# Kernel tuning notes

Measured on AMD Instinct MI355X. Metric: run time of the kernel, lower is better.

Reference implementation:

```python
import jax, jax.numpy as jnp
import numpy as np

N_NODES = 50000
N_EDGES = 800000
EMB = 128
N_LAYERS = 2
BN_EPS = 1e-5


def setup_inputs() -> dict:
    key = jax.random.key(0)
    ks = jax.random.split(key, 16)
    N, E, D, L = N_NODES, N_EDGES, EMB, N_LAYERS
    x = jax.random.randint(ks[0], (N, 2), 0, 3)
    edge_index = jax.random.randint(ks[1], (2, E), 0, N)
    edge_attr = jax.random.randint(ks[2], (E, 2), 0, 3)
    batch = jnp.zeros((N,), dtype=jnp.int32)
    s = 0.1
    xemb1 = jax.random.normal(ks[3], (120, D)) * s   # atom-type embedding
    xemb2 = jax.random.normal(ks[4], (3, D)) * s     # chirality embedding
    e1 = jax.random.normal(ks[5], (L, 7, D)) * s     # bond-type embedding per layer
    e2 = jax.random.normal(ks[6], (L, 3, D)) * s     # bond-direction embedding per layer
    W1 = jax.random.normal(ks[7], (L, D, 2 * D)) * s
    b1 = jnp.zeros((L, 2 * D))
    W2 = jax.random.normal(ks[8], (L, 2 * D, D)) * s
    b2 = jnp.zeros((L, D))
    gamma = jnp.ones((L, D))
    beta = jnp.zeros((L, D))
    return {"x": x, "edge_index": edge_index, "edge_attr": edge_attr, "batch": batch,
            "xemb1": xemb1, "xemb2": xemb2, "e1": e1, "e2": e2,
            "W1": W1, "b1": b1, "W2": W2, "b2": b2, "gamma": gamma, "beta": beta}


def _gnn_forward(x, edge_index, edge_attr, xemb1, xemb2, e1, e2, W1, b1, W2, b2, gamma, beta):
    N = x.shape[0]
    # add self loops; self-loop edge_attr = [4, 0]
    loop = jnp.arange(N, dtype=edge_index.dtype)
    src = jnp.concatenate([edge_index[0], loop])
    dst = jnp.concatenate([edge_index[1], loop])
    loop_attr = jnp.concatenate([jnp.full((N, 1), 4, dtype=edge_attr.dtype),
                                 jnp.zeros((N, 1), dtype=edge_attr.dtype)], axis=1)
    ea = jnp.concatenate([edge_attr, loop_attr], axis=0)  # [E+N, 2]

    # input node embedding
    h = xemb1[x[:, 0]] + xemb2[x[:, 1]]  # [N, D]

    for l in range(N_LAYERS):
        eemb = e1[l][ea[:, 0]] + e2[l][ea[:, 1]]      # [E+N, D]
        msg = h[src] + eemb                            # gather + edge fuse
        agg = jax.ops.segment_sum(msg, dst, num_segments=N)  # scatter-add
        # GIN update MLP: Linear -> ReLU -> Linear
        h2 = jax.nn.relu(agg @ W1[l] + b1[l]) @ W2[l] + b2[l]
        # BatchNorm1d (training mode: biased batch stats)
        mu = jnp.mean(h2, axis=0)
        var = jnp.mean(jnp.square(h2 - mu), axis=0)
        h2 = gamma[l] * (h2 - mu) * jax.lax.rsqrt(var + BN_EPS) + beta[l]
        # dropout(relu) for non-final layers; drop_ratio=0 -> identity dropout
        h = h2 if l == N_LAYERS - 1 else jax.nn.relu(h2)
    return h  # JK='last'


def reference(x, edge_index, edge_attr, batch, xemb1, xemb2, e1, e2, W1, b1, W2, b2, gamma, beta):
    return _gnn_forward(x, edge_index, edge_attr, xemb1, xemb2, e1, e2, W1, b1, W2, b2, gamma, beta)
```

## Files before the change

### kernel.cpp

```cpp
#include <hip/hip_runtime.h>
#include <stdint.h>

#define N_NODES 50000
#define N_EDGES 800000
#define EMB 128
#define NPAD 50176
#define MBLK 392
#define BN_EPS 1e-5f
#define SENT_KEY ((N_NODES << 5) | 21)
#define NODES_PER_XCD 6250
#define XCHUNK 2048
#define NCHUNKS ((N_EDGES + XCHUNK - 1) / XCHUNK)
#define PBLK 196

typedef __attribute__((ext_vector_type(8))) short short8;
typedef __attribute__((ext_vector_type(4))) float f32x4;

__device__ __forceinline__ unsigned short f2bf(float f) {
    unsigned int u = __float_as_uint(f);
    u += 0x7fffu + ((u >> 16) & 1u);
    return (unsigned short)(u >> 16);
}
__device__ __forceinline__ float bflo(unsigned int v) { return __uint_as_float(v << 16); }
__device__ __forceinline__ float bfhi(unsigned int v) { return __uint_as_float(v & 0xffff0000u); }
__device__ __forceinline__ unsigned int packbf(float lo, float hi) {
    return (unsigned int)f2bf(lo) | ((unsigned int)f2bf(hi) << 16);
}

__global__ void k_prep(const int* __restrict__ x, const float* __restrict__ xe1,
                       const float* __restrict__ xe2, unsigned int* __restrict__ h,
                       const float* __restrict__ W1, const float* __restrict__ W2,
                       unsigned short* __restrict__ w1t, unsigned short* __restrict__ w2t,
                       int* __restrict__ deg,
                       const int* __restrict__ ei, const int* __restrict__ ea,
                       int* __restrict__ keyv) {
    int idx = blockIdx.x * 256 + threadIdx.x;
    int i = idx >> 6, j = idx & 63;
    if (i < N_NODES) {
        int a = x[2 * i], c = x[2 * i + 1];
        float2 va = *(const float2*)(xe1 + a * EMB + j * 2);
        float2 vb = *(const float2*)(xe2 + c * EMB + j * 2);
        h[i * 64 + j] = packbf(va.x + vb.x, va.y + vb.y);
    } else if (i == N_NODES) {
        h[(size_t)i * 64 + j] = 0u;
    }
    if (idx < 4 * 32768) {
        int sec = idx >> 15, q = idx & 32767;
        if (sec < 2) {
            int r = q >> 8, c = q & 255;
            w1t[sec * 32768 + c * 128 + r] = f2bf(W1[sec * 32768 + q]);
        } else {
            int s = sec - 2;
            int r = q >> 7, c = q & 127;
            w2t[s * 32768 + c * 256 + r] = f2bf(W2[s * 32768 + q]);
        }
    }
    if (idx < N_EDGES) {
        int2 aa = *(const int2*)(ea + 2 * idx);
        keyv[idx] = (ei[idx] << 5) | (aa.x * 3 + aa.y);
        atomicAdd(&deg[ei[N_EDGES + idx]], 1);
    }
}

__global__ void k_alloc(const int* __restrict__ deg, int* __restrict__ gcur,
                        int* __restrict__ offs, int* __restrict__ cursor,
                        int* __restrict__ keys, int* __restrict__ bcnt) {
    __shared__ int wbase[4];
    __shared__ int lc[8];
    int tid = threadIdx.x, lane = tid & 63, wid = tid >> 6;
    if (tid < 8) lc[tid] = 0;
    int i = blockIdx.x * 256 + tid;
    int d = (i < N_NODES) ? deg[i] : 0;
    int pd = (d + 15) & ~15;
    int s = pd;
#pragma unroll
    for (int off = 1; off < 64; off <<= 1) {
        int t = __shfl_up(s, off);
        if (lane >= off) s += t;
    }
    if (lane == 63) wbase[wid] = s;
    __syncthreads();
    if (tid == 0) {
        int t0 = wbase[0], t1 = wbase[1], t2 = wbase[2], t3 = wbase[3];
        int b = atomicAdd(gcur, t0 + t1 + t2 + t3);
        wbase[0] = b; wbase[1] = b + t0; wbase[2] = b + t0 + t1; wbase[3] = b + t0 + t1 + t2;
    }
    __syncthreads();
    if (i < N_NODES) {
        int o = wbase[wid] + s - pd;
        offs[i] = o;
        cursor[i] = o;
        for (int j = d; j < pd; ++j) keys[o + j] = SENT_KEY;
        int nch = pd >> 4;
        atomicAdd(&lc[nch > 7 ? 7 : nch], 1);
    }
    __syncthreads();
    if (tid < 8) atomicAdd(&bcnt[tid], lc[tid]);
}

__global__ void k_fill(const int* __restrict__ dst, const int* __restrict__ keyv,
                       int* __restrict__ cursor, int* __restrict__ keys,
                       const int* __restrict__ deg, const int* __restrict__ bcnt,
                       int* __restrict__ bcur, int* __restrict__ perm) {
    int xcd = blockIdx.x & 7, chunk = blockIdx.x >> 3;
    int lo = xcd * NODES_PER_XCD, hi = lo + NODES_PER_XCD;
    int e0 = chunk * XCHUNK + threadIdx.x * 4;
#pragma unroll
    for (int it = 0; it < XCHUNK / 1024; ++it) {
        int e = e0 + it * 1024;
        if (e < N_EDGES) {
            int4 d4 = *(const int4*)(dst + e);
            int dv[4] = {d4.x, d4.y, d4.z, d4.w};
#pragma unroll
            for (int q = 0; q < 4; ++q) {
                int d = dv[q];
                if (d >= lo && d < hi) {
                    int p = atomicAdd(&cursor[d], 1);
                    keys[p] = keyv[e + q];
                }
            }
        }
    }
    if (blockIdx.x < PBLK) {
        __shared__ int lcnt[8], gbase[8], tbase[8];
        if (threadIdx.x < 8) lcnt[threadIdx.x] = 0;
        __syncthreads();
        int i = blockIdx.x * 256 + threadIdx.x;
        int b = 0, lrank = 0;
        if (i < N_NODES) {
            int nch = (deg[i] + 15) >> 4;
            b = nch > 7 ? 7 : nch;
            lrank = atomicAdd(&lcnt[b], 1);
        }
        __syncthreads();
        if (threadIdx.x < 8) {
            gbase[threadIdx.x] = atomicAdd(&bcur[threadIdx.x], lcnt[threadIdx.x]);
            int s = 0;
            for (int k = 0; k < threadIdx.x; ++k) s += bcnt[k];
            tbase[threadIdx.x] = s;
        }
        __syncthreads();
        if (i < N_NODES) perm[tbase[b] + gbase[b] + lrank] = i;
    }
}

__global__ __launch_bounds__(256, 4) void k_agg(
    const unsigned int* __restrict__ h,
    const int* __restrict__ offs,
    const int* __restrict__ deg,
    const int* __restrict__ keys,
    const int* __restrict__ perm,
    const float* __restrict__ e1l, const float* __restrict__ e2l,
    unsigned int* __restrict__ agg)
{
    __shared__ float e12[22 * 132];
    for (int t = threadIdx.x; t < 22 * 128; t += 256) {
        int combo = t >> 7, f = t & 127;
        float v = 0.f;
        if (combo < 21) {
            int a0 = combo / 3, a1 = combo - a0 * 3;
            v = e1l[a0 * EMB + f] + e2l[a1 * EMB + f];
        }
        e12[combo * 132 + f] = v;
    }
    __syncthreads();
    int wave = threadIdx.x >> 6, lane = threadIdx.x & 63;
    int sub = lane >> 4, fl = lane & 15;
    int wi = blockIdx.x * 4 + wave;
    int q = (wi & 255) * 49 + (wi >> 8);
    int slot = q * 4 + sub;
    int node = (slot < N_NODES) ? perm[slot] : slot;
    float ax[8] = {0.f, 0.f, 0.f, 0.f, 0.f, 0.f, 0.f, 0.f};
    int o = 0, nch = 0;
    if (node < N_NODES) {
        o = offs[node];
        nch = (deg[node] + 15) >> 4;
        uint4 hv = *(const uint4*)(h + (size_t)node * 64 + fl * 4);
        const float* ep = e12 + 12 * 132 + fl * 8;
        float4 e0 = *(const float4*)ep, e1_ = *(const float4*)(ep + 4);
        ax[0] = bflo(hv.x) + e0.x;  ax[1] = bfhi(hv.x) + e0.y;
        ax[2] = bflo(hv.y) + e0.z;  ax[3] = bfhi(hv.y) + e0.w;
        ax[4] = bflo(hv.z) + e1_.x; ax[5] = bfhi(hv.z) + e1_.y;
        ax[6] = bflo(hv.w) + e1_.z; ax[7] = bfhi(hv.w) + e1_.w;
    }
    int maxch = nch;
#pragma unroll
    for (int d = 32; d; d >>= 1) maxch = max(maxch, __shfl_xor(maxch, d));
    int key = (0 < nch) ? keys[o + fl] : SENT_KEY;
    for (int c = 0; c < maxch; ++c) {
        int keyn = (c + 1 < nch) ? keys[o + (c + 1) * 16 + fl] : SENT_KEY;
        int kjA[8], kjB[8];
        uint4 g[8];
#pragma unroll
        for (int j = 0; j < 8; ++j) {
            kjA[j] = __shfl(key, sub * 16 + j);
            g[j] = *(const uint4*)(h + (size_t)(kjA[j] >> 5) * 64 + fl * 4);
        }
#pragma unroll
        for (int j = 0; j < 8; ++j) {
            uint4 gg = g[j];
            kjB[j] = __shfl(key, sub * 16 + 8 + j);
            g[j] = *(const uint4*)(h + (size_t)(kjB[j] >> 5) * 64 + fl * 4);
            const float* ep = e12 + (kjA[j] & 31) * 132 + fl * 8;
            float4 e0 = *(const float4*)ep, e1_ = *(const float4*)(ep + 4);
            ax[0] += bflo(gg.x) + e0.x;  ax[1] += bfhi(gg.x) + e0.y;
            ax[2] += bflo(gg.y) + e0.z;  ax[3] += bfhi(gg.y) + e0.w;
            ax[4] += bflo(gg.z) + e1_.x; ax[5] += bfhi(gg.z) + e1_.y;
            ax[6] += bflo(gg.w) + e1_.z; ax[7] += bfhi(gg.w) + e1_.w;
        }
#pragma unroll
        for (int j = 0; j < 8; ++j) {
            uint4 gg = g[j];
            const float* ep = e12 + (kjB[j] & 31) * 132 + fl * 8;
            float4 e0 = *(const float4*)ep, e1_ = *(const float4*)(ep + 4);
            ax[0] += bflo(gg.x) + e0.x;  ax[1] += bfhi(gg.x) + e0.y;
            ax[2] += bflo(gg.y) + e0.z;  ax[3] += bfhi(gg.y) + e0.w;
            ax[4] += bflo(gg.z) + e1_.x; ax[5] += bfhi(gg.z) + e1_.y;
            ax[6] += bflo(gg.w) + e1_.z; ax[7] += bfhi(gg.w) + e1_.w;
        }
        key = keyn;
    }
    {
        uint4 out;
        out.x = packbf(ax[0], ax[1]); out.y = packbf(ax[2], ax[3]);
        out.z = packbf(ax[4], ax[5]); out.w = packbf(ax[6], ax[7]);
        *(uint4*)(agg + (size_t)node * 64 + fl * 4) = out;
    }
}

__global__ __launch_bounds__(256, 2) void k_mlp(
    unsigned short* aggh2,
    const unsigned short* __restrict__ w1t,
    const float* __restrict__ b1,
    const unsigned short* __restrict__ w2t,
    const float* __restrict__ b2,
    float* __restrict__ bnsum)
{
    __shared__ float bn[256];
    int lane = threadIdx.x & 63;
    int wave = threadIdx.x >> 6;
    int quad = lane >> 4, r16 = lane & 15;
    int m0 = (blockIdx.x * 4 + wave) * 32;
    int sel  = (lane >> 5) & 1;
    int srcA = ((lane >> 4) & 1) * 32 + r16;
    int srcB = srcA + 16;
    bn[threadIdx.x] = 0.f;

    short8 bagg[2][4];
#pragma unroll
    for (int t = 0; t < 2; ++t)
#pragma unroll
        for (int c = 0; c < 4; ++c)
            bagg[t][c] = *(const short8*)(aggh2 + (size_t)(m0 + t * 16 + r16) * 128 + c * 32 + quad * 8);

    float b2v[8];
#pragma unroll
    for (int n = 0; n < 8; ++n) b2v[n] = b2[n * 16 + r16];

    f32x4 acc2[2][8];
#pragma unroll
    for (int t = 0; t < 2; ++t)
#pragma unroll
        for (int n = 0; n < 8; ++n) acc2[t][n] = (f32x4){0.f, 0.f, 0.f, 0.f};

    for (int c2 = 0; c2 < 8; ++c2) {
        unsigned int pk[2][2][2];
#pragma unroll
        for (int ntl = 0; ntl < 2; ++ntl) {
            int nt = c2 * 2 + ntl;
            short8 aw[4];
#pragma unroll
            for (int c = 0; c < 4; ++c)
                aw[c] = *(const short8*)(w1t + (nt * 16 + r16) * 128 + c * 32 + quad * 8);
            float4 bv = *(const float4*)(b1 + nt * 16 + quad * 4);
#pragma unroll
            for (int t = 0; t < 2; ++t) {
                f32x4 a1 = {0.f, 0.f, 0.f, 0.f};
#pragma unroll
                for (int c = 0; c < 4; ++c)
                    a1 = __builtin_amdgcn_mfma_f32_16x16x32_bf16(aw[c], bagg[t][c], a1, 0, 0, 0);
                float v0 = a1[0] + bv.x; v0 = v0 > 0.f ? v0 : 0.f;
                float v1 = a1[1] + bv.y; v1 = v1 > 0.f ? v1 : 0.f;
                float v2 = a1[2] + bv.z; v2 = v2 > 0.f ? v2 : 0.f;
                float v3 = a1[3] + bv.w; v3 = v3 > 0.f ? v3 : 0.f;
                pk[ntl][t][0] = packbf(v0, v1);
                pk[ntl][t][1] = packbf(v2, v3);
            }
        }
        short8 a2f[2];
#pragma unroll
        for (int t = 0; t < 2; ++t) {
            int u0 = __shfl((int)pk[0][t][0], srcA), w0 = __shfl((int)pk[1][t][0], srcA);
            int u1 = __shfl((int)pk[0][t][1], srcA), w1_ = __shfl((int)pk[1][t][1], srcA);
            int u2 = __shfl((int)pk[0][t][0], srcB), w2_ = __shfl((int)pk[1][t][0], srcB);
            int u3 = __shfl((int)pk[0][t][1], srcB), w3_ = __shfl((int)pk[1][t][1], srcB);
            union { int i[4]; short8 s; } a2u;
            a2u.i[0] = sel ? w0 : u0;
            a2u.i[1] = sel ? w1_ : u1;
            a2u.i[2] = sel ? w2_ : u2;
            a2u.i[3] = sel ? w3_ : u3;
            a2f[t] = a2u.s;
        }
#pragma unroll
        for (int n = 0; n < 8; ++n) {
            short8 bw = *(const short8*)(w2t + (n * 16 + r16) * 256 + c2 * 32 + quad * 8);
            acc2[0][n] = __builtin_amdgcn_mfma_f32_16x16x32_bf16(a2f[0], bw, acc2[0][n], 0, 0, 0);
            acc2[1][n] = __builtin_amdgcn_mfma_f32_16x16x32_bf16(a2f[1], bw, acc2[1][n], 0, 0, 0);
        }
    }
    float s[8], q[8];
#pragma unroll
    for (int n = 0; n < 8; ++n) { s[n] = 0.f; q[n] = 0.f; }
#pragma unroll
    for (int t = 0; t < 2; ++t)
#pragma unroll
        for (int n = 0; n < 8; ++n)
#pragma unroll
            for (int r = 0; r < 4; ++r) {
                int row = m0 + t * 16 + quad * 4 + r;
                float v = acc2[t][n][r] + b2v[n];
                if (row < N_NODES) {
                    aggh2[(size_t)row * 128 + n * 16 + r16] = f2bf(v);
                    s[n] += v; q[n] += v * v;
                }
            }
#pragma unroll
    for (int n = 0; n < 8; ++n) {
        s[n] += __shfl_xor(s[n], 16); q[n] += __shfl_xor(q[n], 16);
        s[n] += __shfl_xor(s[n], 32); q[n] += __shfl_xor(q[n], 32);
    }
    __syncthreads();
    if (quad == 0) {
#pragma unroll
        for (int n = 0; n < 8; ++n) {
            atomicAdd(&bn[n * 16 + r16], s[n]);
            atomicAdd(&bn[128 + n * 16 + r16], q[n]);
        }
    }
    __syncthreads();
    atomicAdd(&bnsum[threadIdx.x], bn[threadIdx.x]);
}

__global__ void k_bnnorm(const uint4* __restrict__ h2, const float* __restrict__ bnsum,
                         const float* __restrict__ gamma, const float* __restrict__ beta,
                         uint4* __restrict__ outb, float4* __restrict__ outf, int mode) {
    __shared__ float ab[256];
    int tid = threadIdx.x;
    if (tid < 128) {
        float mean = bnsum[tid] * (1.f / N_NODES);
        float var  = bnsum[128 + tid] * (1.f / N_NODES) - mean * mean;
        float rstd = rsqrtf(var + BN_EPS);
        float g = gamma[tid];
        ab[tid]       = g * rstd;
        ab[128 + tid] = beta[tid] - mean * g * rstd;
    }
    __syncthreads();
    int idx = blockIdx.x * 256 + tid;
    if (idx >= N_NODES * 16) return;
    int p = (idx & 15) * 8;
    uint4 hv = h2[idx];
    float v0 = bflo(hv.x) * ab[p + 0] + ab[128 + p + 0];
    float v1 = bfhi(hv.x) * ab[p + 1] + ab[128 + p + 1];
    float v2 = bflo(hv.y) * ab[p + 2] + ab[128 + p + 2];
    float v3 = bfhi(hv.y) * ab[p + 3] + ab[128 + p + 3];
    float v4 = bflo(hv.z) * ab[p + 4] + ab[128 + p + 4];
    float v5 = bfhi(hv.z) * ab[p + 5] + ab[128 + p + 5];
    float v6 = bflo(hv.w) * ab[p + 6] + ab[128 + p + 6];
    float v7 = bfhi(hv.w) * ab[p + 7] + ab[128 + p + 7];
    if (mode == 0) {
        v0 = v0 > 0.f ? v0 : 0.f; v1 = v1 > 0.f ? v1 : 0.f;
        v2 = v2 > 0.f ? v2 : 0.f; v3 = v3 > 0.f ? v3 : 0.f;
        v4 = v4 > 0.f ? v4 : 0.f; v5 = v5 > 0.f ? v5 : 0.f;
        v6 = v6 > 0.f ? v6 : 0.f; v7 = v7 > 0.f ? v7 : 0.f;
        uint4 out;
        out.x = packbf(v0, v1); out.y = packbf(v2, v3);
        out.z = packbf(v4, v5); out.w = packbf(v6, v7);
        outb[idx] = out;
    } else {
        outf[2 * idx]     = make_float4(v0, v1, v2, v3);
        outf[2 * idx + 1] = make_float4(v4, v5, v6, v7);
    }
}

extern "C" void kernel_launch(void* const* d_in, const int* in_sizes, int n_in,
                              void* d_out, int out_size, void* d_ws, size_t ws_size,
                              hipStream_t stream) {
    const int* x  = (const int*)d_in[0];
    const int* ei = (const int*)d_in[1];
    const int* ea = (const int*)d_in[2];
    const float* xe1 = (const float*)d_in[4];
    const float* xe2 = (const float*)d_in[5];
    const float* e1  = (const float*)d_in[6];
    const float* e2  = (const float*)d_in[7];
    const float* W1  = (const float*)d_in[8];
    const float* b1  = (const float*)d_in[9];
    const float* W2  = (const float*)d_in[10];
    const float* b2  = (const float*)d_in[11];
    const float* gm  = (const float*)d_in[12];
    const float* bt  = (const float*)d_in[13];

    char* ws = (char*)d_ws;
    size_t off = 0;
    auto take = [&](size_t bytes) -> char* {
        char* p = ws + off;
        off = (off + bytes + 255) & ~(size_t)255;
        return p;
    };
    unsigned int* h_buf = (unsigned int*)take((size_t)(N_NODES + 1) * 64 * 4);
    unsigned int* aggb  = (unsigned int*)take((size_t)NPAD * 64 * 4);
    unsigned short* w1t = (unsigned short*)take((size_t)2 * 32768 * 2);
    unsigned short* w2t = (unsigned short*)take((size_t)2 * 32768 * 2);
    int* zbuf   = (int*)take((size_t)(N_NODES + 512 + 32) * 4);
    int* deg    = zbuf;
    float* bnsum = (float*)(zbuf + N_NODES);
    int* bmeta  = zbuf + N_NODES + 512;
    int* offs   = (int*)take((size_t)(N_NODES + 1) * 4);
    int* cursor = (int*)take((size_t)N_NODES * 4);
    int* keys   = (int*)take((size_t)(N_EDGES + N_NODES * 16) * 4);
    int* keyv   = (int*)take((size_t)N_EDGES * 4);
    int* perm   = (int*)take((size_t)N_NODES * 4);
    int* bcnt = bmeta, *bcur = bmeta + 8, *gcur = bmeta + 16;

    hipMemsetAsync(zbuf, 0, (size_t)(N_NODES + 512 + 32) * 4, stream);
    k_prep<<<((N_NODES + 1) * 64 + 255) / 256, 256, 0, stream>>>(x, xe1, xe2, h_buf,
                                                                 W1, W2, w1t, w2t, deg,
                                                                 ei, ea, keyv);
    k_alloc<<<PBLK, 256, 0, stream>>>(deg, gcur, offs, cursor, keys, bcnt);
    k_fill<<<8 * NCHUNKS, 256, 0, stream>>>(ei + N_EDGES, keyv, cursor, keys,
                                            deg, bcnt, bcur, perm);

    for (int l = 0; l < 2; ++l) {
        k_agg<<<NPAD / 16, 256, 0, stream>>>(h_buf, offs, deg, keys, perm,
                                             e1 + l * 896, e2 + l * 384, aggb);
        k_mlp<<<MBLK, 256, 0, stream>>>((unsigned short*)aggb, w1t + l * 32768, b1 + l * 256,
                                        w2t + l * 32768, b2 + l * 128, bnsum + l * 256);
        k_bnnorm<<<(N_NODES * 16 + 255) / 256, 256, 0, stream>>>((const uint4*)aggb, bnsum + l * 256,
                                                                 gm + l * 128, bt + l * 128,
                                                                 (uint4*)h_buf, (float4*)d_out, l);
    }
}
```

Baseline: 365.6 us.

## Fold edge embeddings into first MLP matmul via per-node combo counts

Edge-embedding contributions are now computed algebraically instead of inside aggregation: per-node counts of the 21 bond-attribute combos are accumulated with atomics in prep, converted to bf16, and multiplied by a precomputed (e1+e2)@W1 table as an extra K=32 MFMA slice in the MLP. This removes the shared-memory embedding table build and the per-edge embedding loads and adds from the gather loop. In exchange it adds 800k extra atomics into a 4.2MB count array, a larger memset, and a small extra MFMA per tile. Counts and the projected table are rounded to bf16, which slightly changes precision.

After: 384.6 us. 5.2% more time.

```diff
diff --git a/kernel.cpp b/kernel.cpp
--- a/kernel.cpp
+++ b/kernel.cpp
@@ -33,7 +33,7 @@
                        unsigned short* __restrict__ w1t, unsigned short* __restrict__ w2t,
                        int* __restrict__ deg,
                        const int* __restrict__ ei, const int* __restrict__ ea,
-                       int* __restrict__ keyv) {
+                       int* __restrict__ keyv, int* __restrict__ cnt32) {
     int idx = blockIdx.x * 256 + threadIdx.x;
     int i = idx >> 6, j = idx & 63;
     if (i < N_NODES) {
@@ -57,14 +57,20 @@
     }
     if (idx < N_EDGES) {
         int2 aa = *(const int2*)(ea + 2 * idx);
-        keyv[idx] = (ei[idx] << 5) | (aa.x * 3 + aa.y);
-        atomicAdd(&deg[ei[N_EDGES + idx]], 1);
+        int combo = aa.x * 3 + aa.y;
+        keyv[idx] = (ei[idx] << 5) | combo;
+        int d = ei[N_EDGES + idx];
+        atomicAdd(&deg[d], 1);
+        atomicAdd(&cnt32[d * 21 + combo], 1);
     }
 }
 
 __global__ void k_alloc(const int* __restrict__ deg, int* __restrict__ gcur,
                         int* __restrict__ offs, int* __restrict__ cursor,
-                        int* __restrict__ keys, int* __restrict__ bcnt) {
+                        int* __restrict__ keys, int* __restrict__ bcnt,
+                        const int* __restrict__ cnt32, unsigned short* __restrict__ cntb,
+                        const float* __restrict__ e1, const float* __restrict__ e2,
+                        const float* __restrict__ W1, unsigned short* __restrict__ w1e) {
     __shared__ int wbase[4];
     __shared__ int lc[8];
     int tid = threadIdx.x, lane = tid & 63, wid = tid >> 6;
@@ -96,6 +102,41 @@
     }
     __syncthreads();
     if (tid < 8) atomicAdd(&bcnt[tid], lc[tid]);
+
+    {
+        unsigned int pk_[16];
+#pragma unroll
+        for (int w = 0; w < 16; ++w) pk_[w] = 0;
+        if (i < N_NODES) {
+#pragma unroll
+            for (int cc = 0; cc < 21; ++cc) {
+                int v = cnt32[i * 21 + cc] + (cc == 12 ? 1 : 0);
+                unsigned int b = (unsigned int)f2bf((float)v);
+                pk_[cc >> 1] |= b << ((cc & 1) * 16);
+            }
+        }
+        uint4* dst4 = (uint4*)(cntb + (size_t)i * 32);
+        dst4[0] = make_uint4(pk_[0], pk_[1], pk_[2], pk_[3]);
+        dst4[1] = make_uint4(pk_[4], pk_[5], pk_[6], pk_[7]);
+        dst4[2] = make_uint4(pk_[8], pk_[9], pk_[10], pk_[11]);
+        dst4[3] = make_uint4(pk_[12], pk_[13], pk_[14], pk_[15]);
+    }
+
+    if (blockIdx.x < 42) {
+        int l = blockIdx.x / 21, c = blockIdx.x % 21;
+        int a0 = c / 3, a1 = c - a0 * 3;
+        const float* E1 = e1 + l * 896 + a0 * 128;
+        const float* E2 = e2 + l * 384 + a1 * 128;
+        const float* w1 = W1 + l * 32768;
+        int n = tid;
+        float acc = 0.f;
+        for (int k = 0; k < 128; ++k)
+            acc = fmaf(E1[k] + E2[k], w1[k * 256 + n], acc);
+        w1e[(size_t)l * 8192 + n * 32 + c] = f2bf(acc);
+        if (c == 0) {
+            for (int cc = 21; cc < 32; ++cc) w1e[(size_t)l * 8192 + n * 32 + cc] = 0;
+        }
+    }
 }
 
 __global__ void k_fill(const int* __restrict__ dst, const int* __restrict__ keyv,
@@ -150,20 +191,8 @@
     const int* __restrict__ deg,
     const int* __restrict__ keys,
     const int* __restrict__ perm,
-    const float* __restrict__ e1l, const float* __restrict__ e2l,
     unsigned int* __restrict__ agg)
 {
-    __shared__ float e12[22 * 132];
-    for (int t = threadIdx.x; t < 22 * 128; t += 256) {
-        int combo = t >> 7, f = t & 127;
-        float v = 0.f;
-        if (combo < 21) {
-            int a0 = combo / 3, a1 = combo - a0 * 3;
-            v = e1l[a0 * EMB + f] + e2l[a1 * EMB + f];
-        }
-        e12[combo * 132 + f] = v;
-    }
-    __syncthreads();
     int wave = threadIdx.x >> 6, lane = threadIdx.x & 63;
     int sub = lane >> 4, fl = lane & 15;
     int wi = blockIdx.x * 4 + wave;
@@ -176,12 +205,10 @@
         o = offs[node];
         nch = (deg[node] + 15) >> 4;
         uint4 hv = *(const uint4*)(h + (size_t)node * 64 + fl * 4);
-        const float* ep = e12 + 12 * 132 + fl * 8;
-        float4 e0 = *(const float4*)ep, e1_ = *(const float4*)(ep + 4);
-        ax[0] = bflo(hv.x) + e0.x;  ax[1] = bfhi(hv.x) + e0.y;
-        ax[2] = bflo(hv.y) + e0.z;  ax[3] = bfhi(hv.y) + e0.w;
-        ax[4] = bflo(hv.z) + e1_.x; ax[5] = bfhi(hv.z) + e1_.y;
-        ax[6] = bflo(hv.w) + e1_.z; ax[7] = bfhi(hv.w) + e1_.w;
+        ax[0] = bflo(hv.x);  ax[1] = bfhi(hv.x);
+        ax[2] = bflo(hv.y);  ax[3] = bfhi(hv.y);
+        ax[4] = bflo(hv.z);  ax[5] = bfhi(hv.z);
+        ax[6] = bflo(hv.w);  ax[7] = bfhi(hv.w);
     }
     int maxch = nch;
 #pragma unroll
@@ -189,34 +216,29 @@
     int key = (0 < nch) ? keys[o + fl] : SENT_KEY;
     for (int c = 0; c < maxch; ++c) {
         int keyn = (c + 1 < nch) ? keys[o + (c + 1) * 16 + fl] : SENT_KEY;
-        int kjA[8], kjB[8];
         uint4 g[8];
 #pragma unroll
         for (int j = 0; j < 8; ++j) {
-            kjA[j] = __shfl(key, sub * 16 + j);
-            g[j] = *(const uint4*)(h + (size_t)(kjA[j] >> 5) * 64 + fl * 4);
+            int kj = __shfl(key, sub * 16 + j);
+            g[j] = *(const uint4*)(h + (size_t)(kj >> 5) * 64 + fl * 4);
         }
 #pragma unroll
         for (int j = 0; j < 8; ++j) {
             uint4 gg = g[j];
-            kjB[j] = __shfl(key, sub * 16 + 8 + j);
-            g[j] = *(const uint4*)(h + (size_t)(kjB[j] >> 5) * 64 + fl * 4);
-            const float* ep = e12 + (kjA[j] & 31) * 132 + fl * 8;
-            float4 e0 = *(const float4*)ep, e1_ = *(const float4*)(ep + 4);
-            ax[0] += bflo(gg.x) + e0.x;  ax[1] += bfhi(gg.x) + e0.y;
-            ax[2] += bflo(gg.y) + e0.z;  ax[3] += bfhi(gg.y) + e0.w;
-            ax[4] += bflo(gg.z) + e1_.x; ax[5] += bfhi(gg.z) + e1_.y;
-            ax[6] += bflo(gg.w) + e1_.z; ax[7] += bfhi(gg.w) + e1_.w;
+            int kb = __shfl(key, sub * 16 + 8 + j);
+            g[j] = *(const uint4*)(h + (size_t)(kb >> 5) * 64 + fl * 4);
+            ax[0] += bflo(gg.x);  ax[1] += bfhi(gg.x);
+            ax[2] += bflo(gg.y);  ax[3] += bfhi(gg.y);
+            ax[4] += bflo(gg.z);  ax[5] += bfhi(gg.z);
+            ax[6] += bflo(gg.w);  ax[7] += bfhi(gg.w);
         }
 #pragma unroll
         for (int j = 0; j < 8; ++j) {
             uint4 gg = g[j];
-            const float* ep = e12 + (kjB[j] & 31) * 132 + fl * 8;
-            float4 e0 = *(const float4*)ep, e1_ = *(const float4*)(ep + 4);
-            ax[0] += bflo(gg.x) + e0.x;  ax[1] += bfhi(gg.x) + e0.y;
-            ax[2] += bflo(gg.y) + e0.z;  ax[3] += bfhi(gg.y) + e0.w;
-            ax[4] += bflo(gg.z) + e1_.x; ax[5] += bfhi(gg.z) + e1_.y;
-            ax[6] += bflo(gg.w) + e1_.z; ax[7] += bfhi(gg.w) + e1_.w;
+            ax[0] += bflo(gg.x);  ax[1] += bfhi(gg.x);
+            ax[2] += bflo(gg.y);  ax[3] += bfhi(gg.y);
+            ax[4] += bflo(gg.z);  ax[5] += bfhi(gg.z);
+            ax[6] += bflo(gg.w);  ax[7] += bfhi(gg.w);
         }
         key = keyn;
     }
@@ -230,7 +252,9 @@
 
 __global__ __launch_bounds__(256, 2) void k_mlp(
     unsigned short* aggh2,
+    const unsigned short* __restrict__ cntb,
     const unsigned short* __restrict__ w1t,
+    const unsigned short* __restrict__ w1e,
     const float* __restrict__ b1,
     const unsigned short* __restrict__ w2t,
     const float* __restrict__ b2,
@@ -246,12 +270,14 @@
     int srcB = srcA + 16;
     bn[threadIdx.x] = 0.f;
 
-    short8 bagg[2][4];
-#pragma unroll
-    for (int t = 0; t < 2; ++t)
+    short8 bagg[2][5];
+#pragma unroll
+    for (int t = 0; t < 2; ++t) {
 #pragma unroll
         for (int c = 0; c < 4; ++c)
             bagg[t][c] = *(const short8*)(aggh2 + (size_t)(m0 + t * 16 + r16) * 128 + c * 32 + quad * 8);
+        bagg[t][4] = *(const short8*)(cntb + (size_t)(m0 + t * 16 + r16) * 32 + quad * 8);
+    }
 
     float b2v[8];
 #pragma unroll
@@ -268,16 +294,17 @@
 #pragma unroll
         for (int ntl = 0; ntl < 2; ++ntl) {
             int nt = c2 * 2 + ntl;
-            short8 aw[4];
+            short8 aw[5];
 #pragma unroll
             for (int c = 0; c < 4; ++c)
                 aw[c] = *(const short8*)(w1t + (nt * 16 + r16) * 128 + c * 32 + quad * 8);
+            aw[4] = *(const short8*)(w1e + (nt * 16 + r16) * 32 + quad * 8);
             float4 bv = *(const float4*)(b1 + nt * 16 + quad * 4);
 #pragma unroll
             for (int t = 0; t < 2; ++t) {
                 f32x4 a1 = {0.f, 0.f, 0.f, 0.f};
 #pragma unroll
-                for (int c = 0; c < 4; ++c)
+                for (int c = 0; c < 5; ++c)
                     a1 = __builtin_amdgcn_mfma_f32_16x16x32_bf16(aw[c], bagg[t][c], a1, 0, 0, 0);
                 float v0 = a1[0] + bv.x; v0 = v0 > 0.f ? v0 : 0.f;
                 float v1 = a1[1] + bv.y; v1 = v1 > 0.f ? v1 : 0.f;
@@ -410,10 +437,13 @@
     unsigned int* aggb  = (unsigned int*)take((size_t)NPAD * 64 * 4);
     unsigned short* w1t = (unsigned short*)take((size_t)2 * 32768 * 2);
     unsigned short* w2t = (unsigned short*)take((size_t)2 * 32768 * 2);
-    int* zbuf   = (int*)take((size_t)(N_NODES + 512 + 32) * 4);
+    unsigned short* w1e = (unsigned short*)take((size_t)2 * 8192 * 2);
+    unsigned short* cntb = (unsigned short*)take((size_t)NPAD * 32 * 2);
+    int* zbuf   = (int*)take((size_t)(N_NODES + 512 + 32 + (size_t)N_NODES * 21) * 4);
     int* deg    = zbuf;
     float* bnsum = (float*)(zbuf + N_NODES);
     int* bmeta  = zbuf + N_NODES + 512;
+    int* cnt32  = zbuf + N_NODES + 512 + 32;
     int* offs   = (int*)take((size_t)(N_NODES + 1) * 4);
     int* cursor = (int*)take((size_t)N_NODES * 4);
     int* keys   = (int*)take((size_t)(N_EDGES + N_NODES * 16) * 4);
@@ -421,18 +451,19 @@
     int* perm   = (int*)take((size_t)N_NODES * 4);
     int* bcnt = bmeta, *bcur = bmeta + 8, *gcur = bmeta + 16;
 
-    hipMemsetAsync(zbuf, 0, (size_t)(N_NODES + 512 + 32) * 4, stream);
+    hipMemsetAsync(zbuf, 0, (size_t)(N_NODES + 512 + 32 + (size_t)N_NODES * 21) * 4, stream);
     k_prep<<<((N_NODES + 1) * 64 + 255) / 256, 256, 0, stream>>>(x, xe1, xe2, h_buf,
                                                                  W1, W2, w1t, w2t, deg,
-                                                                 ei, ea, keyv);
-    k_alloc<<<PBLK, 256, 0, stream>>>(deg, gcur, offs, cursor, keys, bcnt);
+                                                                 ei, ea, keyv, cnt32);
+    k_alloc<<<PBLK, 256, 0, stream>>>(deg, gcur, offs, cursor, keys, bcnt,
+                                      cnt32, cntb, e1, e2, W1, w1e);
     k_fill<<<8 * NCHUNKS, 256, 0, stream>>>(ei + N_EDGES, keyv, cursor, keys,
                                             deg, bcnt, bcur, perm);
 
     for (int l = 0; l < 2; ++l) {
-        k_agg<<<NPAD / 16, 256, 0, stream>>>(h_buf, offs, deg, keys, perm,
-                                             e1 + l * 896, e2 + l * 384, aggb);
-        k_mlp<<<MBLK, 256, 0, stream>>>((unsigned short*)aggb, w1t + l * 32768, b1 + l * 256,
+        k_agg<<<NPAD / 16, 256, 0, stream>>>(h_buf, offs, deg, keys, perm, aggb);
+        k_mlp<<<MBLK, 256, 0, stream>>>((unsigned short*)aggb, cntb,
+                                        w1t + l * 32768, w1e + l * 8192, b1 + l * 256,
                                         w2t + l * 32768, b2 + l * 128, bnsum + l * 256);
         k_bnnorm<<<(N_NODES * 16 + 255) / 256, 256, 0, stream>>>((const uint4*)aggb, bnsum + l * 256,
                                                                  gm + l * 128, bt + l * 128,
```
